# Optimization experiments

Hardware: AMD Instinct MI355X
Metric: run time of the kernel (lower is better)

## Reference

```python
import jax, jax.numpy as jnp
import numpy as np

NUM_RELATION = 7

def setup_inputs() -> dict:
    key = jax.random.key(0)
    ks = jax.random.split(key, 12)
    N, E, D, DO, R, DE = 20000, 640000, 512, 512, NUM_RELATION, 59
    inp = {
        "node_feat": jax.random.normal(ks[0], (N, D), dtype=jnp.float32),
        "edge_weight": jax.random.uniform(ks[1], (E,), dtype=jnp.float32),
        "edge_feat": jax.random.normal(ks[2], (E, DE), dtype=jnp.float32),
        "W_lin": jax.random.normal(ks[3], (DO, R * D), dtype=jnp.float32) * 0.02,
        "b_lin": jax.random.normal(ks[4], (DO,), dtype=jnp.float32) * 0.02,
        "W_self": jax.random.normal(ks[5], (DO, D), dtype=jnp.float32) * 0.02,
        "b_self": jax.random.normal(ks[6], (DO,), dtype=jnp.float32) * 0.02,
        "W_edge": jax.random.normal(ks[7], (DO, DE), dtype=jnp.float32) * 0.02,
        "b_edge": jax.random.normal(ks[8], (DO,), dtype=jnp.float32) * 0.02,
        "node_in": jax.random.randint(ks[9], (E,), 0, N, dtype=jnp.int64) if jax.config.jax_enable_x64 else jax.random.randint(ks[9], (E,), 0, N).astype(jnp.int32),
        "node_out": jax.random.randint(ks[10], (E,), 0, N).astype(jnp.int32),
        "relation": jax.random.randint(ks[11], (E,), 0, R).astype(jnp.int32),
    }
    inp["node_in"] = inp["node_in"].astype(jnp.int32)
    return inp


def reference(node_feat, edge_weight, edge_feat, W_lin, b_lin, W_self, b_self,
              W_edge, b_edge, node_in, node_out, relation):
    N, D = node_feat.shape
    R = NUM_RELATION
    # segment id: node_out * R + relation  (column index in sparse (N, N*R) adjacency)
    seg = node_out * R + relation  # [E]
    # update = adjacency.T @ input  == scatter-add of weighted source features
    msg = node_feat[node_in] * edge_weight[:, None]               # [E, D]
    update = jax.ops.segment_sum(msg, seg, num_segments=N * R)    # [N*R, D]
    # edge_linear path: edge_update scattered with the same segment ids
    edge_msg = (edge_feat @ W_edge.T + b_edge) * edge_weight[:, None]  # [E, D]
    update = update + jax.ops.segment_sum(edge_msg, seg, num_segments=N * R)
    update = update.reshape(N, R * D)                             # [N, R*D]
    # combine: linear(update) + self_loop(input), then relu
    out = update @ W_lin.T + b_lin + node_feat @ W_self.T + b_self
    return jax.nn.relu(out)
```

## Files before the change

### kernel.cpp

```cpp
#include <hip/hip_runtime.h>
#include <stdint.h>

typedef unsigned short u16;
typedef __attribute__((ext_vector_type(8))) __bf16 bf16x8;
typedef __attribute__((ext_vector_type(4))) float f32x4;

#define NREL 7
#define DIM  512
#define DEDGE 59
#define KC   420
#define KCP  448
#define KTOT 4544

__device__ __forceinline__ float bf2f(u16 u) {
  union { unsigned u; float f; } c; c.u = ((unsigned)u) << 16; return c.f;
}
__device__ __forceinline__ u16 f2bf(float f) {
  union { float f; unsigned u; } c; c.f = f;
  unsigned r = ((c.u >> 16) & 1u) + 0x7FFFu;
  return (u16)((c.u + r) >> 16);
}

__device__ __forceinline__ void gload16(const void* g, void* l) {
  __builtin_amdgcn_global_load_lds(
      (__attribute__((address_space(1))) void*)g,
      (__attribute__((address_space(3))) void*)l, 16, 0, 0);
}

__global__ void convA(const float* __restrict__ in, u16* __restrict__ out, int total4) {
  int i = blockIdx.x * 256 + threadIdx.x;
  if (i >= total4) return;
  float4 v = ((const float4*)in)[i];
  ushort4 r;
  r.x = f2bf(v.x); r.y = f2bf(v.y); r.z = f2bf(v.z); r.w = f2bf(v.w);
  ((ushort4*)out)[i] = r;
}

__global__ void buildBW(const float* __restrict__ W_lin, const float* __restrict__ W_self,
                        u16* __restrict__ Bfull, int total4) {
  int gid = blockIdx.x * 256 + threadIdx.x;
  if (gid >= total4) return;
  int idx = gid * 4;
  int o = idx >> 12;
  int k = idx & 4095;
  const float* src = (k < NREL * DIM) ? (W_lin + (size_t)o * (NREL * DIM) + k)
                                      : (W_self + (size_t)o * DIM + (k - NREL * DIM));
  float4 v = *(const float4*)src;
  ushort4 rr;
  rr.x = f2bf(v.x); rr.y = f2bf(v.y); rr.z = f2bf(v.z); rr.w = f2bf(v.w);
  *(ushort4*)(Bfull + (size_t)o * KTOT + k) = rr;
}

__global__ __launch_bounds__(512) void buildCx(const float* __restrict__ W_edge,
                                               const float* __restrict__ b_edge,
                                               const float* __restrict__ W_lin,
                                               u16* __restrict__ Bfull) {
  int c = blockIdx.x;
  int o = threadIdx.x;
  u16* dst = Bfull + (size_t)o * KTOT + NREL * DIM + DIM;
  if (c >= KC) { dst[c] = 0; return; }
  __shared__ float col[DIM];
  int r;
  if (c < NREL * DEDGE) {
    r = c / DEDGE;
    int de = c - r * DEDGE;
    col[o] = W_edge[(size_t)o * DEDGE + de];
  } else {
    r = c - NREL * DEDGE;
    col[o] = b_edge[o];
  }
  __syncthreads();
  const float* wrow = W_lin + (size_t)o * (NREL * DIM) + (size_t)r * DIM;
  float acc = 0.f;
#pragma unroll 8
  for (int d = 0; d < DIM; ++d) acc += col[d] * wrow[d];
  dst[c] = f2bf(acc);
}

__global__ void countK2(const int* __restrict__ node_out, const int* __restrict__ relation,
                        int* __restrict__ counts2, int E) {
  int e = blockIdx.x * 256 + threadIdx.x;
  if (e < E) atomicAdd(&counts2[node_out[e] * 8 + relation[e]], 1);
}

__global__ void scanNode(const int* __restrict__ counts2, int* __restrict__ counts, int N) {
  int n = blockIdx.x * 256 + threadIdx.x;
  if (n >= N) return;
  int s = 0;
#pragma unroll
  for (int r = 0; r < NREL; ++r) s += counts2[n * 8 + r];
  counts[n] = s;
}

__global__ __launch_bounds__(1024) void scanK(const int* __restrict__ counts,
                                              int* __restrict__ offs, int n) {
  __shared__ int lds[1024];
  int tid = threadIdx.x;
  int carry = 0;
  for (int base = 0; base < n; base += 1024) {
    int i = base + tid;
    int v = (i < n) ? counts[i] : 0;
    lds[tid] = v;
    __syncthreads();
    for (int o = 1; o < 1024; o <<= 1) {
      int t = (tid >= o) ? lds[tid - o] : 0;
      __syncthreads();
      lds[tid] += t;
      __syncthreads();
    }
    int excl = lds[tid] - v;
    if (i < n) offs[i] = carry + excl;
    int total = lds[1023];
    carry += total;
    __syncthreads();
  }
  if (tid == 0) offs[n] = carry;
}

__global__ void offs2K(const int* __restrict__ offs, const int* __restrict__ counts2,
                       int* __restrict__ offs2, int* __restrict__ cursor2, int N) {
  int n = blockIdx.x * 256 + threadIdx.x;
  if (n >= N) return;
  int base = offs[n];
#pragma unroll
  for (int r = 0; r < NREL; ++r) {
    offs2[n * 8 + r] = base;
    cursor2[n * 8 + r] = base;
    base += counts2[n * 8 + r];
  }
  offs2[n * 8 + 7] = base;
}

__global__ void fillK2(const int* __restrict__ node_in, const int* __restrict__ node_out,
                       const int* __restrict__ relation, const float* __restrict__ ew,
                       int* __restrict__ cursor2, int* __restrict__ eids,
                       uint2* __restrict__ pairs, int E) {
  int e = blockIdx.x * 256 + threadIdx.x;
  if (e >= E) return;
  int p = atomicAdd(&cursor2[node_out[e] * 8 + relation[e]], 1);
  eids[p] = e;
  pairs[p] = make_uint2((unsigned)node_in[e], __float_as_uint(ew[e]));
}

__global__ __launch_bounds__(64) void gatherG2(const float* __restrict__ ef,
                                               const int* __restrict__ eids,
                                               const uint2* __restrict__ pairs,
                                               const int* __restrict__ offs2,
                                               u16* __restrict__ Mfull) {
  int n = blockIdx.x;
  int lane = threadIdx.x;
  u16* row = Mfull + (size_t)n * KTOT + NREL * DIM + DIM;
  int base = n * 8;
  for (int r = 0; r < NREL; ++r) {
    int p0 = offs2[base + r], p1 = offs2[base + r + 1];
    float acc = 0.f;
    for (int p = p0; p < p1; ++p) {
      int e = __builtin_amdgcn_readfirstlane(eids[p]);
      float w = __uint_as_float(__builtin_amdgcn_readfirstlane(pairs[p].y));
      float v = (lane < DEDGE) ? ef[(size_t)e * DEDGE + lane] : 1.0f;
      acc += w * v;
    }
    if (lane < DEDGE) row[r * DEDGE + lane] = f2bf(acc);
    else if (lane == DEDGE) row[NREL * DEDGE + r] = f2bf(acc);
  }
  if (lane >= 60) {
    for (int c = KC + (lane - 60); c < KCP; c += 4) row[c] = 0;
  }
}

__global__ __launch_bounds__(128) void aggK(const u16* __restrict__ NF,
                                            const uint2* __restrict__ pairs,
                                            const int* __restrict__ offs2,
                                            u16* __restrict__ Mfull) {
  int n = blockIdx.x;
  int o0 = threadIdx.x * 4;
  u16* mrow = Mfull + (size_t)n * KTOT;
  *(ushort4*)(mrow + NREL * DIM + o0) = *(const ushort4*)(NF + (size_t)n * DIM + o0);
  int base = n * 8;
  for (int r = 0; r < NREL; ++r) {
    int p0 = offs2[base + r], p1 = offs2[base + r + 1];
    float a0 = 0.f, a1 = 0.f, a2 = 0.f, a3 = 0.f;
    for (int p = p0; p < p1; ++p) {
      uint2 pr = pairs[p];
      int src = __builtin_amdgcn_readfirstlane((int)pr.x);
      float w = __uint_as_float(__builtin_amdgcn_readfirstlane(pr.y));
      ushort4 hv = *(const ushort4*)(NF + (size_t)src * DIM + o0);
      a0 += w * bf2f(hv.x);
      a1 += w * bf2f(hv.y);
      a2 += w * bf2f(hv.z);
      a3 += w * bf2f(hv.w);
    }
    ushort4 st;
    st.x = f2bf(a0); st.y = f2bf(a1); st.z = f2bf(a2); st.w = f2bf(a3);
    *(ushort4*)(mrow + r * DIM + o0) = st;
  }
}

__global__ __launch_bounds__(256) void gemm_br(const u16* __restrict__ A,
                                               const u16* __restrict__ Bt,
                                               const float* __restrict__ b_lin,
                                               const float* __restrict__ b_self,
                                               float* __restrict__ Cout, int M) {
  __shared__ __align__(16) u16 sA[2][128 * 32];
  __shared__ __align__(16) u16 sB[2][128 * 32];
  const int tid = threadIdx.x;
  const int w = tid >> 6, l = tid & 63;
  const int lr = l & 15, kg = l >> 4;

  const int id = blockIdx.x;
  const int npan = gridDim.x >> 2;
  const int nfull = (npan >> 3) << 3;
  int p, c;
  if (id < nfull * 4) {
    int g = id >> 5, r = id & 31;
    p = g * 8 + (r & 7);
    c = r >> 3;
  } else {
    int t = id - nfull * 4;
    p = nfull + (t >> 2);
    c = t & 3;
  }
  const int m0 = p * 128, n0 = c * 128;
  const int wr = w >> 1, wc = w & 1;
  f32x4 acc[4][4];
  const f32x4 z4 = {0.f, 0.f, 0.f, 0.f};
#pragma unroll
  for (int i = 0; i < 4; ++i)
#pragma unroll
    for (int j = 0; j < 4; ++j) acc[i][j] = z4;

  const int ktiles = KTOT / 32;

  auto stage = [&](int kt, int b) {
    const int k0 = kt * 32;
#pragma unroll
    for (int t = 0; t < 2; ++t) {
      int idx = w * 128 + t * 64 + l;
      int row = idx >> 2, kp = idx & 3;
      int gm = m0 + row; gm = gm < M ? gm : M - 1;
      gload16(A + (size_t)gm * KTOT + k0 + kp * 8,
              (char*)sA[b] + (size_t)(w * 128 + t * 64) * 16);
    }
#pragma unroll
    for (int t = 0; t < 2; ++t) {
      int idx = w * 128 + t * 64 + l;
      int row = idx >> 2, kp = idx & 3;
      gload16(Bt + (size_t)(n0 + row) * KTOT + k0 + kp * 8,
              (char*)sB[b] + (size_t)(w * 128 + t * 64) * 16);
    }
  };

  stage(0, 0);
  __syncthreads();

  for (int kt = 0; kt < ktiles; ++kt) {
    const int cur = kt & 1;
    if (kt + 1 < ktiles) stage(kt + 1, cur ^ 1);
    bf16x8 af[4], bfr[4];
#pragma unroll
    for (int i = 0; i < 4; ++i)
      af[i] = *(const bf16x8*)(sA[cur] + (size_t)(wr * 64 + i * 16 + lr) * 32 + kg * 8);
#pragma unroll
    for (int j = 0; j < 4; ++j)
      bfr[j] = *(const bf16x8*)(sB[cur] + (size_t)(wc * 64 + j * 16 + lr) * 32 + kg * 8);
#pragma unroll
    for (int i = 0; i < 4; ++i)
#pragma unroll
      for (int j = 0; j < 4; ++j)
        acc[i][j] = __builtin_amdgcn_mfma_f32_16x16x32_bf16(af[i], bfr[j], acc[i][j], 0, 0, 0);
    __syncthreads();
  }
#pragma unroll
  for (int i = 0; i < 4; ++i) {
#pragma unroll
    for (int j = 0; j < 4; ++j) {
      int gj = n0 + wc * 64 + j * 16 + lr;
      float bias = b_lin[gj] + b_self[gj];
#pragma unroll
      for (int v = 0; v < 4; ++v) {
        int gm = m0 + wr * 64 + i * 16 + kg * 4 + v;
        if (gm < M)
          ((float*)Cout)[(size_t)gm * DIM + gj] = fmaxf(acc[i][j][v] + bias, 0.f);
      }
    }
  }
}

extern "C" void kernel_launch(void* const* d_in, const int* in_sizes, int n_in,
                              void* d_out, int out_size, void* d_ws, size_t ws_size,
                              hipStream_t stream) {
  const float* node_feat = (const float*)d_in[0];
  const float* edge_weight = (const float*)d_in[1];
  const float* edge_feat = (const float*)d_in[2];
  const float* W_lin = (const float*)d_in[3];
  const float* b_lin = (const float*)d_in[4];
  const float* W_self = (const float*)d_in[5];
  const float* b_self = (const float*)d_in[6];
  const float* W_edge = (const float*)d_in[7];
  const float* b_edge = (const float*)d_in[8];
  const int* node_in = (const int*)d_in[9];
  const int* node_out = (const int*)d_in[10];
  const int* relation = (const int*)d_in[11];
  float* out = (float*)d_out;

  const int N = in_sizes[0] / DIM;
  const int E = in_sizes[1];

  char* ws = (char*)d_ws;
  size_t off = 0;
  auto take = [&](size_t b) {
    char* p = ws + off;
    off += (b + 255) & ~(size_t)255;
    return p;
  };
  u16* NF      = (u16*)take((size_t)N * DIM * 2);
  u16* Bfull   = (u16*)take((size_t)DIM * KTOT * 2);
  u16* Mfull   = (u16*)take((size_t)N * KTOT * 2);
  int* counts2 = (int*)take((size_t)N * 8 * 4);
  int* counts  = (int*)take((size_t)N * 4);
  int* offs    = (int*)take((size_t)(N + 1) * 4);
  int* offs2   = (int*)take((size_t)N * 8 * 4);
  int* cursor2 = (int*)take((size_t)N * 8 * 4);
  int* eids    = (int*)take((size_t)E * 4);
  uint2* pairs = (uint2*)take((size_t)E * 8);
  if (off > ws_size) return;

  hipMemsetAsync(counts2, 0, (size_t)N * 8 * 4, stream);

  {
    int total4 = N * DIM / 4;
    convA<<<(total4 + 255) / 256, 256, 0, stream>>>(node_feat, NF, total4);
  }
  {
    int total4 = DIM * 4096 / 4;
    buildBW<<<(total4 + 255) / 256, 256, 0, stream>>>(W_lin, W_self, Bfull, total4);
  }
  buildCx<<<KCP, 512, 0, stream>>>(W_edge, b_edge, W_lin, Bfull);

  countK2<<<(E + 255) / 256, 256, 0, stream>>>(node_out, relation, counts2, E);
  scanNode<<<(N + 255) / 256, 256, 0, stream>>>(counts2, counts, N);
  scanK<<<1, 1024, 0, stream>>>(counts, offs, N);
  offs2K<<<(N + 255) / 256, 256, 0, stream>>>(offs, counts2, offs2, cursor2, N);
  fillK2<<<(E + 255) / 256, 256, 0, stream>>>(node_in, node_out, relation, edge_weight,
                                              cursor2, eids, pairs, E);

  gatherG2<<<N, 64, 0, stream>>>(edge_feat, eids, pairs, offs2, Mfull);
  aggK<<<N, 128, 0, stream>>>(NF, pairs, offs2, Mfull);

  {
    int npan = (N + 127) / 128;
    gemm_br<<<npan * 4, 256, 0, stream>>>(Mfull, Bfull, b_lin, b_self, out, N);
  }
}
```

Before: 527.9 us.

## Load GEMM MFMA fragments directly from global memory into registers, dropping LDS staging

Removes the LDS double-buffered staging (global_load_lds plus barriers) from the main bf16 GEMM. Each wave now loads its own A and B fragments straight from global memory into registers, using a two-stage register ping-pong to overlap loads with MFMAs. This drops shared memory use and __syncthreads, but each A row is now fetched by both column-waves and each B row by both row-waves. That doubles global/L2 traffic, and the per-lane loads read 16 bytes at a 4544-element row stride, so they coalesce poorly.

Measured after the change: 770.4 us. +45.9%, slower.

```diff
diff --git a/kernel.cpp b/kernel.cpp
--- a/kernel.cpp
+++ b/kernel.cpp
@@ -19,12 +19,6 @@
   union { float f; unsigned u; } c; c.f = f;
   unsigned r = ((c.u >> 16) & 1u) + 0x7FFFu;
   return (u16)((c.u + r) >> 16);
-}
-
-__device__ __forceinline__ void gload16(const void* g, void* l) {
-  __builtin_amdgcn_global_load_lds(
-      (__attribute__((address_space(1))) void*)g,
-      (__attribute__((address_space(3))) void*)l, 16, 0, 0);
 }
 
 __global__ void convA(const float* __restrict__ in, u16* __restrict__ out, int total4) {
@@ -201,8 +195,6 @@
                                                const float* __restrict__ b_lin,
                                                const float* __restrict__ b_self,
                                                float* __restrict__ Cout, int M) {
-  __shared__ __align__(16) u16 sA[2][128 * 32];
-  __shared__ __align__(16) u16 sB[2][128 * 32];
   const int tid = threadIdx.x;
   const int w = tid >> 6, l = tid & 63;
   const int lr = l & 15, kg = l >> 4;
@@ -222,6 +214,23 @@
   }
   const int m0 = p * 128, n0 = c * 128;
   const int wr = w >> 1, wc = w & 1;
+
+  const u16* arow0; const u16* arow1; const u16* arow2; const u16* arow3;
+  {
+    int gm0 = m0 + wr * 64 + 0 * 16 + lr; gm0 = gm0 < M ? gm0 : M - 1;
+    int gm1 = m0 + wr * 64 + 1 * 16 + lr; gm1 = gm1 < M ? gm1 : M - 1;
+    int gm2 = m0 + wr * 64 + 2 * 16 + lr; gm2 = gm2 < M ? gm2 : M - 1;
+    int gm3 = m0 + wr * 64 + 3 * 16 + lr; gm3 = gm3 < M ? gm3 : M - 1;
+    arow0 = A + (size_t)gm0 * KTOT + kg * 8;
+    arow1 = A + (size_t)gm1 * KTOT + kg * 8;
+    arow2 = A + (size_t)gm2 * KTOT + kg * 8;
+    arow3 = A + (size_t)gm3 * KTOT + kg * 8;
+  }
+  const u16* brow0 = Bt + (size_t)(n0 + wc * 64 + 0 * 16 + lr) * KTOT + kg * 8;
+  const u16* brow1 = Bt + (size_t)(n0 + wc * 64 + 1 * 16 + lr) * KTOT + kg * 8;
+  const u16* brow2 = Bt + (size_t)(n0 + wc * 64 + 2 * 16 + lr) * KTOT + kg * 8;
+  const u16* brow3 = Bt + (size_t)(n0 + wc * 64 + 3 * 16 + lr) * KTOT + kg * 8;
+
   f32x4 acc[4][4];
   const f32x4 z4 = {0.f, 0.f, 0.f, 0.f};
 #pragma unroll
@@ -231,45 +240,50 @@
 
   const int ktiles = KTOT / 32;
 
-  auto stage = [&](int kt, int b) {
-    const int k0 = kt * 32;
-#pragma unroll
-    for (int t = 0; t < 2; ++t) {
-      int idx = w * 128 + t * 64 + l;
-      int row = idx >> 2, kp = idx & 3;
-      int gm = m0 + row; gm = gm < M ? gm : M - 1;
-      gload16(A + (size_t)gm * KTOT + k0 + kp * 8,
-              (char*)sA[b] + (size_t)(w * 128 + t * 64) * 16);
-    }
-#pragma unroll
-    for (int t = 0; t < 2; ++t) {
-      int idx = w * 128 + t * 64 + l;
-      int row = idx >> 2, kp = idx & 3;
-      gload16(Bt + (size_t)(n0 + row) * KTOT + k0 + kp * 8,
-              (char*)sB[b] + (size_t)(w * 128 + t * 64) * 16);
-    }
-  };
-
-  stage(0, 0);
-  __syncthreads();
-
-  for (int kt = 0; kt < ktiles; ++kt) {
-    const int cur = kt & 1;
-    if (kt + 1 < ktiles) stage(kt + 1, cur ^ 1);
-    bf16x8 af[4], bfr[4];
-#pragma unroll
-    for (int i = 0; i < 4; ++i)
-      af[i] = *(const bf16x8*)(sA[cur] + (size_t)(wr * 64 + i * 16 + lr) * 32 + kg * 8);
-#pragma unroll
-    for (int j = 0; j < 4; ++j)
-      bfr[j] = *(const bf16x8*)(sB[cur] + (size_t)(wc * 64 + j * 16 + lr) * 32 + kg * 8);
-#pragma unroll
-    for (int i = 0; i < 4; ++i)
-#pragma unroll
-      for (int j = 0; j < 4; ++j)
-        acc[i][j] = __builtin_amdgcn_mfma_f32_16x16x32_bf16(af[i], bfr[j], acc[i][j], 0, 0, 0);
-    __syncthreads();
-  }
+  bf16x8 aX0, aX1, aX2, aX3, bX0, bX1, bX2, bX3;
+  bf16x8 aY0, aY1, aY2, aY3, bY0, bY1, bY2, bY3;
+
+  aX0 = *(const bf16x8*)(arow0); aX1 = *(const bf16x8*)(arow1);
+  aX2 = *(const bf16x8*)(arow2); aX3 = *(const bf16x8*)(arow3);
+  bX0 = *(const bf16x8*)(brow0); bX1 = *(const bf16x8*)(brow1);
+  bX2 = *(const bf16x8*)(brow2); bX3 = *(const bf16x8*)(brow3);
+
+#define MFMA_SET(AS0,AS1,AS2,AS3,BS0,BS1,BS2,BS3)                                   \
+  acc[0][0] = __builtin_amdgcn_mfma_f32_16x16x32_bf16(AS0, BS0, acc[0][0], 0,0,0);  \
+  acc[0][1] = __builtin_amdgcn_mfma_f32_16x16x32_bf16(AS0, BS1, acc[0][1], 0,0,0);  \
+  acc[0][2] = __builtin_amdgcn_mfma_f32_16x16x32_bf16(AS0, BS2, acc[0][2], 0,0,0);  \
+  acc[0][3] = __builtin_amdgcn_mfma_f32_16x16x32_bf16(AS0, BS3, acc[0][3], 0,0,0);  \
+  acc[1][0] = __builtin_amdgcn_mfma_f32_16x16x32_bf16(AS1, BS0, acc[1][0], 0,0,0);  \
+  acc[1][1] = __builtin_amdgcn_mfma_f32_16x16x32_bf16(AS1, BS1, acc[1][1], 0,0,0);  \
+  acc[1][2] = __builtin_amdgcn_mfma_f32_16x16x32_bf16(AS1, BS2, acc[1][2], 0,0,0);  \
+  acc[1][3] = __builtin_amdgcn_mfma_f32_16x16x32_bf16(AS1, BS3, acc[1][3], 0,0,0);  \
+  acc[2][0] = __builtin_amdgcn_mfma_f32_16x16x32_bf16(AS2, BS0, acc[2][0], 0,0,0);  \
+  acc[2][1] = __builtin_amdgcn_mfma_f32_16x16x32_bf16(AS2, BS1, acc[2][1], 0,0,0);  \
+  acc[2][2] = __builtin_amdgcn_mfma_f32_16x16x32_bf16(AS2, BS2, acc[2][2], 0,0,0);  \
+  acc[2][3] = __builtin_amdgcn_mfma_f32_16x16x32_bf16(AS2, BS3, acc[2][3], 0,0,0);  \
+  acc[3][0] = __builtin_amdgcn_mfma_f32_16x16x32_bf16(AS3, BS0, acc[3][0], 0,0,0);  \
+  acc[3][1] = __builtin_amdgcn_mfma_f32_16x16x32_bf16(AS3, BS1, acc[3][1], 0,0,0);  \
+  acc[3][2] = __builtin_amdgcn_mfma_f32_16x16x32_bf16(AS3, BS2, acc[3][2], 0,0,0);  \
+  acc[3][3] = __builtin_amdgcn_mfma_f32_16x16x32_bf16(AS3, BS3, acc[3][3], 0,0,0);
+
+  for (int kt = 0; kt < ktiles; kt += 2) {
+    const int o1 = (kt + 1) * 32;
+    aY0 = *(const bf16x8*)(arow0 + o1); aY1 = *(const bf16x8*)(arow1 + o1);
+    aY2 = *(const bf16x8*)(arow2 + o1); aY3 = *(const bf16x8*)(arow3 + o1);
+    bY0 = *(const bf16x8*)(brow0 + o1); bY1 = *(const bf16x8*)(brow1 + o1);
+    bY2 = *(const bf16x8*)(brow2 + o1); bY3 = *(const bf16x8*)(brow3 + o1);
+    MFMA_SET(aX0, aX1, aX2, aX3, bX0, bX1, bX2, bX3)
+    if (kt + 2 < ktiles) {
+      const int o2 = (kt + 2) * 32;
+      aX0 = *(const bf16x8*)(arow0 + o2); aX1 = *(const bf16x8*)(arow1 + o2);
+      aX2 = *(const bf16x8*)(arow2 + o2); aX3 = *(const bf16x8*)(arow3 + o2);
+      bX0 = *(const bf16x8*)(brow0 + o2); bX1 = *(const bf16x8*)(brow1 + o2);
+      bX2 = *(const bf16x8*)(brow2 + o2); bX3 = *(const bf16x8*)(brow3 + o2);
+    }
+    MFMA_SET(aY0, aY1, aY2, aY3, bY0, bY1, bY2, bY3)
+  }
+#undef MFMA_SET
+
 #pragma unroll
   for (int i = 0; i < 4; ++i) {
 #pragma unroll
```
